# Optimization experiments

Hardware: AMD Instinct MI355X
Metric: run time of the kernel (lower is better)

Reference implementation:

```python
import jax, jax.numpy as jnp
import numpy as np

B, C, D = 4096, 1000, 3072


def setup_inputs() -> dict:
    key = jax.random.key(0)
    k1, k2, k3, k4 = jax.random.split(key, 4)
    scale = 1.0
    return {
        "z": jax.random.normal(k1, (B, D), dtype=jnp.float32),
        "sldj": jax.random.normal(k2, (B,), dtype=jnp.float32),
        "labels": jax.random.randint(k3, (B,), 0, C),
        "beta": jnp.ones((), dtype=jnp.float32),
        "means": jax.random.normal(k4, (C, D), dtype=jnp.float32) * scale,
    }


def reference(z, sldj, labels, beta, means):
    # dists[i,j] = -0.5 * ||z_i - mu_j||^2, via a^2 + b^2 - 2ab GEMM trick
    z2 = jnp.sum(z * z, axis=1, keepdims=True)          # [B,1]
    m2 = jnp.sum(means * means, axis=1)[None, :]        # [1,C]
    cross = jnp.einsum('bd,cd->bc', z, means)           # [B,C] GEMM
    dists = -0.5 * (z2 + m2 - 2.0 * cross)              # [B,C]

    log_pz = jax.nn.logsumexp(dists, axis=1)            # [B]
    # cross_entropy(dists, labels) = mean(logsumexp - dists[i, y_i])
    picked = jnp.take_along_axis(dists, labels[:, None], axis=1)[:, 0]
    loss_cls = jnp.mean(log_pz - picked)
    loss_gen = -jnp.mean(log_pz + sldj) / z.shape[1]
    total = loss_gen + beta * loss_cls
    return total, loss_gen, loss_cls
```

## Files before the change

kernel.cpp:

```cpp
#include <hip/hip_runtime.h>
#include <hip/hip_bf16.h>
#include <cstdint>
#include <cstddef>

#define NB 4096
#define NC 1000
#define NCP 1024
#define ND 3072

typedef __attribute__((ext_vector_type(8))) __bf16 bf16x8;
typedef __attribute__((ext_vector_type(4))) float f32x4;
typedef __attribute__((ext_vector_type(4))) unsigned short u16x4;
typedef unsigned short u16;

__device__ __forceinline__ u16 f2bf_rne(float x) {
    uint32_t u = __float_as_uint(x);
    uint32_t r = (u + 0x7fffu + ((u >> 16) & 1u)) >> 16;
    return (u16)r;
}

__global__ __launch_bounds__(256) void convert_rows_kernel(
        const float* __restrict__ src, u16* __restrict__ dst,
        float* __restrict__ sq, int nrows_src, float pad_sq) {
    const int row = blockIdx.x;
    const int tid = threadIdx.x;
    u16* drow = dst + (size_t)row * ND;
    if (row < nrows_src) {
        const float4* s = (const float4*)(src + (size_t)row * ND);
        float acc = 0.f;
#pragma unroll
        for (int i = 0; i < 3; ++i) {
            const int idx = tid + i * 256;
            float4 v = s[idx];
            acc = fmaf(v.x, v.x, acc);
            acc = fmaf(v.y, v.y, acc);
            acc = fmaf(v.z, v.z, acc);
            acc = fmaf(v.w, v.w, acc);
            u16x4 o;
            o.x = f2bf_rne(v.x); o.y = f2bf_rne(v.y);
            o.z = f2bf_rne(v.z); o.w = f2bf_rne(v.w);
            *(u16x4*)(drow + idx * 4) = o;
        }
#pragma unroll
        for (int off = 32; off > 0; off >>= 1) acc += __shfl_xor(acc, off, 64);
        __shared__ float ssum[4];
        const int wid = tid >> 6, lane = tid & 63;
        if (lane == 0) ssum[wid] = acc;
        __syncthreads();
        if (tid == 0) sq[row] = ssum[0] + ssum[1] + ssum[2] + ssum[3];
    } else {
        u16x4 z4 = (u16x4){0, 0, 0, 0};
#pragma unroll
        for (int i = 0; i < 3; ++i) *(u16x4*)(drow + (tid + i * 256) * 4) = z4;
        if (tid == 0) sq[row] = pad_sq;
    }
}

#define BM 128
#define BN 64
#define BK 64

#define GLOAD_LDS16(gp, lp)                                            \
    __builtin_amdgcn_global_load_lds(                                  \
        (const __attribute__((address_space(1))) void*)(gp),           \
        (__attribute__((address_space(3))) void*)(lp), 16, 0, 0)

__global__ __launch_bounds__(256) void gemm_dists_kernel(
        const u16* __restrict__ zb, const u16* __restrict__ mb,
        const float* __restrict__ z2, const float* __restrict__ m2,
        float* __restrict__ dists) {
    __shared__ u16 As[BM * BK];
    __shared__ u16 Bs[BN * BK];

    const int tid  = threadIdx.x;
    const int wid  = tid >> 6;
    const int lane = tid & 63;
    const int wr   = wid >> 1;
    const int wc   = wid & 1;
    const int lrow = lane & 15;
    const int kgrp = lane >> 4;

    const int nwg = gridDim.x * gridDim.y;
    const int bid = blockIdx.y * gridDim.x + blockIdx.x;
    const int swz = (bid & 7) * (nwg >> 3) + (bid >> 3);
    const int bxg = swz % gridDim.x;
    const int byg = swz / gridDim.x;

    const int brow = byg * BM;
    const int bcol = bxg * BN;

    f32x4 acc[4][2];
#pragma unroll
    for (int m = 0; m < 4; ++m)
#pragma unroll
        for (int n = 0; n < 2; ++n) acc[m][n] = (f32x4){0.f, 0.f, 0.f, 0.f};

    const u16* gA[4];
    u16* lA[4];
#pragma unroll
    for (int g = 0; g < 4; ++g) {
        const int c = g * 256 + tid;
        const int r = c >> 3, p = c & 7, s = p ^ (r & 7);
        gA[g] = zb + (size_t)(brow + r) * ND + s * 8;
        lA[g] = As + (g * 256 + wid * 64) * 8;
    }
    const u16* gB[2];
    u16* lB[2];
#pragma unroll
    for (int g = 0; g < 2; ++g) {
        const int c = g * 256 + tid;
        const int r = c >> 3, p = c & 7, s = p ^ (r & 7);
        gB[g] = mb + (size_t)(bcol + r) * ND + s * 8;
        lB[g] = Bs + (g * 256 + wid * 64) * 8;
    }

    const int lx = lrow & 7;

    for (int k0 = 0; k0 < ND; k0 += BK) {
        __syncthreads();
#pragma unroll
        for (int g = 0; g < 4; ++g) GLOAD_LDS16(gA[g] + k0, lA[g]);
#pragma unroll
        for (int g = 0; g < 2; ++g) GLOAD_LDS16(gB[g] + k0, lB[g]);
        __syncthreads();

#pragma unroll
        for (int ks = 0; ks < 2; ++ks) {
            const int pk = (ks * 4 + kgrp) ^ lx;
            bf16x8 a[4], b[2];
#pragma unroll
            for (int m = 0; m < 4; ++m)
                a[m] = *(const bf16x8*)&As[(wr * 64 + m * 16 + lrow) * BK + pk * 8];
#pragma unroll
            for (int n = 0; n < 2; ++n)
                b[n] = *(const bf16x8*)&Bs[(wc * 32 + n * 16 + lrow) * BK + pk * 8];
#pragma unroll
            for (int m = 0; m < 4; ++m)
#pragma unroll
                for (int n = 0; n < 2; ++n)
                    acc[m][n] = __builtin_amdgcn_mfma_f32_16x16x32_bf16(
                        a[m], b[n], acc[m][n], 0, 0, 0);
        }
    }

#pragma unroll
    for (int n = 0; n < 2; ++n) {
        const int gcol = bcol + wc * 32 + n * 16 + lrow;
        const float mhalf = 0.5f * m2[gcol];
#pragma unroll
        for (int m = 0; m < 4; ++m) {
#pragma unroll
            for (int r = 0; r < 4; ++r) {
                const int grow = brow + wr * 64 + m * 16 + kgrp * 4 + r;
                dists[(size_t)grow * NCP + gcol] =
                    acc[m][n][r] - 0.5f * z2[grow] - mhalf;
            }
        }
    }
}

__global__ __launch_bounds__(256) void row_lse_kernel(
        const float* __restrict__ dists, const int* __restrict__ labels,
        const float* __restrict__ sldj, float* __restrict__ outA,
        float* __restrict__ outB) {
    const int row = blockIdx.x;
    const int tid = threadIdx.x;
    const float* dr = dists + (size_t)row * NCP;
    float4 v = ((const float4*)dr)[tid];

    float mx = fmaxf(fmaxf(v.x, v.y), fmaxf(v.z, v.w));
#pragma unroll
    for (int off = 32; off > 0; off >>= 1) mx = fmaxf(mx, __shfl_xor(mx, off, 64));
    __shared__ float smax[4], ssum[4];
    const int wid = tid >> 6, lane = tid & 63;
    if (lane == 0) smax[wid] = mx;
    __syncthreads();
    const float bm = fmaxf(fmaxf(smax[0], smax[1]), fmaxf(smax[2], smax[3]));

    float s = expf(v.x - bm) + expf(v.y - bm) + expf(v.z - bm) + expf(v.w - bm);
#pragma unroll
    for (int off = 32; off > 0; off >>= 1) s += __shfl_xor(s, off, 64);
    if (lane == 0) ssum[wid] = s;
    __syncthreads();
    if (tid == 0) {
        const float tot = ssum[0] + ssum[1] + ssum[2] + ssum[3];
        const float lpz = bm + logf(tot);
        const float picked = dr[labels[row]];
        outA[row] = lpz - picked;
        outB[row] = lpz + sldj[row];
    }
}

__global__ __launch_bounds__(1024) void finalize_kernel(
        const float* __restrict__ a, const float* __restrict__ b,
        const float* __restrict__ beta, float* __restrict__ out) {
    __shared__ float sa[1024], sb[1024];
    const int tid = threadIdx.x;
    float va = 0.f, vb = 0.f;
    for (int i = tid; i < NB; i += 1024) { va += a[i]; vb += b[i]; }
    sa[tid] = va; sb[tid] = vb;
    __syncthreads();
    for (int s = 512; s > 0; s >>= 1) {
        if (tid < s) { sa[tid] += sa[tid + s]; sb[tid] += sb[tid + s]; }
        __syncthreads();
    }
    if (tid == 0) {
        const float loss_cls = sa[0] / (float)NB;
        const float loss_gen = -(sb[0] / (float)NB) / (float)ND;
        const float total = loss_gen + beta[0] * loss_cls;
        out[0] = total;
        out[1] = loss_gen;
        out[2] = loss_cls;
    }
}

extern "C" void kernel_launch(void* const* d_in, const int* in_sizes, int n_in,
                              void* d_out, int out_size, void* d_ws, size_t ws_size,
                              hipStream_t stream) {
    const float* z      = (const float*)d_in[0];
    const float* sldj   = (const float*)d_in[1];
    const int*   labels = (const int*)d_in[2];
    const float* beta   = (const float*)d_in[3];
    const float* means  = (const float*)d_in[4];
    float* out = (float*)d_out;

    char* ws = (char*)d_ws;
    size_t off = 0;
    u16* zb = (u16*)(ws + off);      off += (size_t)NB * ND * 2;
    u16* mb = (u16*)(ws + off);      off += (size_t)NCP * ND * 2;
    float* z2 = (float*)(ws + off);  off += (size_t)NB * 4;
    float* m2 = (float*)(ws + off);  off += (size_t)NCP * 4;
    float* dists = (float*)(ws + off); off += (size_t)NB * NCP * 4;
    float* ra = (float*)(ws + off);  off += (size_t)NB * 4;
    float* rb = (float*)(ws + off);  off += (size_t)NB * 4;

    convert_rows_kernel<<<NB, 256, 0, stream>>>(z, zb, z2, NB, 0.f);
    convert_rows_kernel<<<NCP, 256, 0, stream>>>(means, mb, m2, NC, 1e30f);
    gemm_dists_kernel<<<dim3(NCP / BN, NB / BM), 256, 0, stream>>>(zb, mb, z2, m2, dists);
    row_lse_kernel<<<NB, 256, 0, stream>>>(dists, labels, sldj, ra, rb);
    finalize_kernel<<<1, 1024, 0, stream>>>(ra, rb, beta, out);
}
```

Baseline: 68.51 us.

## Enlarge GEMM tile to 128x128 and double-buffer LDS loads

Raises the GEMM output tile from 128x64 to 128x128, so each wave computes a 64x64 sub-tile with 16 MFMA accumulators. The k-loop is double-buffered so the global-to-LDS loads for the next k-block are issued before the current block is computed, with one barrier per iteration. The grid swizzle is hardcoded for 8 column tiles and 32 row tiles. The aim is more reuse per loaded byte and hiding load latency. The costs are twice the LDS and more accumulator registers, which may lower occupancy, and only 256 workgroups are launched.

Result: slower. 88.24 us (+28.8%).

```diff
diff --git a/kernel.cpp b/kernel.cpp
--- a/kernel.cpp
+++ b/kernel.cpp
@@ -57,8 +57,11 @@
 }
 
 #define BM 128
-#define BN 64
+#define BN 128
 #define BK 64
+#define KITERS (ND / BK)
+#define ABUF (BM * BK)
+#define BBUF (BN * BK)
 
 #define GLOAD_LDS16(gp, lp)                                            \
     __builtin_amdgcn_global_load_lds(                                  \
@@ -69,8 +72,8 @@
         const u16* __restrict__ zb, const u16* __restrict__ mb,
         const float* __restrict__ z2, const float* __restrict__ m2,
         float* __restrict__ dists) {
-    __shared__ u16 As[BM * BK];
-    __shared__ u16 Bs[BN * BK];
+    __shared__ u16 As[2 * ABUF];
+    __shared__ u16 Bs[2 * BBUF];
 
     const int tid  = threadIdx.x;
     const int wid  = tid >> 6;
@@ -80,72 +83,72 @@
     const int lrow = lane & 15;
     const int kgrp = lane >> 4;
 
-    const int nwg = gridDim.x * gridDim.y;
     const int bid = blockIdx.y * gridDim.x + blockIdx.x;
-    const int swz = (bid & 7) * (nwg >> 3) + (bid >> 3);
-    const int bxg = swz % gridDim.x;
-    const int byg = swz / gridDim.x;
-
-    const int brow = byg * BM;
-    const int bcol = bxg * BN;
-
-    f32x4 acc[4][2];
+    const int swz = (bid & 7) * 32 + (bid >> 3);
+    const int brow = (swz >> 3) * BM;
+    const int bcol = (swz & 7) * BN;
+
+    f32x4 acc[4][4];
 #pragma unroll
     for (int m = 0; m < 4; ++m)
 #pragma unroll
-        for (int n = 0; n < 2; ++n) acc[m][n] = (f32x4){0.f, 0.f, 0.f, 0.f};
-
-    const u16* gA[4];
-    u16* lA[4];
+        for (int n = 0; n < 4; ++n) acc[m][n] = (f32x4){0.f, 0.f, 0.f, 0.f};
+
+    const u16* gA[4]; const u16* gB[4];
+    u16* lA[4];       u16* lB[4];
 #pragma unroll
     for (int g = 0; g < 4; ++g) {
         const int c = g * 256 + tid;
         const int r = c >> 3, p = c & 7, s = p ^ (r & 7);
         gA[g] = zb + (size_t)(brow + r) * ND + s * 8;
+        gB[g] = mb + (size_t)(bcol + r) * ND + s * 8;
         lA[g] = As + (g * 256 + wid * 64) * 8;
-    }
-    const u16* gB[2];
-    u16* lB[2];
-#pragma unroll
-    for (int g = 0; g < 2; ++g) {
-        const int c = g * 256 + tid;
-        const int r = c >> 3, p = c & 7, s = p ^ (r & 7);
-        gB[g] = mb + (size_t)(bcol + r) * ND + s * 8;
         lB[g] = Bs + (g * 256 + wid * 64) * 8;
     }
 
     const int lx = lrow & 7;
 
-    for (int k0 = 0; k0 < ND; k0 += BK) {
-        __syncthreads();
-#pragma unroll
-        for (int g = 0; g < 4; ++g) GLOAD_LDS16(gA[g] + k0, lA[g]);
-#pragma unroll
-        for (int g = 0; g < 2; ++g) GLOAD_LDS16(gB[g] + k0, lB[g]);
-        __syncthreads();
-
+#pragma unroll
+    for (int g = 0; g < 4; ++g) GLOAD_LDS16(gA[g], lA[g]);
+#pragma unroll
+    for (int g = 0; g < 4; ++g) GLOAD_LDS16(gB[g], lB[g]);
+    __syncthreads();
+
+    for (int t = 0; t < KITERS; ++t) {
+        if (t + 1 < KITERS) {
+            const int nb = (t + 1) & 1;
+            const int k0 = (t + 1) * BK;
+#pragma unroll
+            for (int g = 0; g < 4; ++g) GLOAD_LDS16(gA[g] + k0, lA[g] + nb * ABUF);
+#pragma unroll
+            for (int g = 0; g < 4; ++g) GLOAD_LDS16(gB[g] + k0, lB[g] + nb * BBUF);
+        }
+        const int cb = t & 1;
+        const u16* Ac = As + cb * ABUF;
+        const u16* Bc = Bs + cb * BBUF;
 #pragma unroll
         for (int ks = 0; ks < 2; ++ks) {
             const int pk = (ks * 4 + kgrp) ^ lx;
-            bf16x8 a[4], b[2];
+            bf16x8 a[4], b[4];
 #pragma unroll
             for (int m = 0; m < 4; ++m)
-                a[m] = *(const bf16x8*)&As[(wr * 64 + m * 16 + lrow) * BK + pk * 8];
-#pragma unroll
-            for (int n = 0; n < 2; ++n)
-                b[n] = *(const bf16x8*)&Bs[(wc * 32 + n * 16 + lrow) * BK + pk * 8];
+                a[m] = *(const bf16x8*)&Ac[(wr * 64 + m * 16 + lrow) * BK + pk * 8];
+#pragma unroll
+            for (int n = 0; n < 4; ++n)
+                b[n] = *(const bf16x8*)&Bc[(wc * 64 + n * 16 + lrow) * BK + pk * 8];
 #pragma unroll
             for (int m = 0; m < 4; ++m)
 #pragma unroll
-                for (int n = 0; n < 2; ++n)
+                for (int n = 0; n < 4; ++n)
                     acc[m][n] = __builtin_amdgcn_mfma_f32_16x16x32_bf16(
                         a[m], b[n], acc[m][n], 0, 0, 0);
         }
-    }
-
-#pragma unroll
-    for (int n = 0; n < 2; ++n) {
-        const int gcol = bcol + wc * 32 + n * 16 + lrow;
+        __syncthreads();
+    }
+
+#pragma unroll
+    for (int n = 0; n < 4; ++n) {
+        const int gcol = bcol + wc * 64 + n * 16 + lrow;
         const float mhalf = 0.5f * m2[gcol];
 #pragma unroll
         for (int m = 0; m < 4; ++m) {
```
